# Optimization experiments

Hardware: AMD Instinct MI355X
Metric: run time of the kernel (lower is better)

## Reference

```python
import jax, jax.numpy as jnp
import numpy as np

V = 32000   # vocab
H = 512     # hidden = embed dim
L = 2       # lstm layers
S = 64      # source length
K = 3       # beam width
T = 50      # max decode length
BOS = 1


def lstm_cell(x, h, c, Wih, Whh, b):
    # x,h,c: [B,H]; Wih/Whh: [4H,H]; b: [4H]
    z = x @ Wih.T + h @ Whh.T + b
    i, f, g, o = jnp.split(z, 4, axis=-1)
    c = jax.nn.sigmoid(f) * c + jax.nn.sigmoid(i) * jnp.tanh(g)
    h = jax.nn.sigmoid(o) * jnp.tanh(c)
    return h, c


def run_layer(x, Wih, Whh, b):
    # x: [S,B,H] -> outputs [S,B,H], final h,c [B,H]
    B = x.shape[1]
    z = jnp.zeros((B, H), x.dtype)
    def step(carry, xt):
        h, c = carry
        h, c = lstm_cell(xt, h, c, Wih, Whh, b)
        return (h, c), h
    (h, c), ys = jax.lax.scan(step, (z, z), x)
    return ys, h, c


def setup_inputs() -> dict:
    key = jax.random.key(0)
    ks = jax.random.split(key, 10)
    def p(k, shape, s=0.05):
        return jax.random.normal(k, shape, dtype=jnp.float32) * s
    return {
        'input_seq': jax.random.randint(ks[0], (S, 1), 0, V),
        'emb_enc': p(ks[1], (V, H), 0.1),
        'Wih_enc': p(ks[2], (L, 4 * H, H)),
        'Whh_enc': p(ks[3], (L, 4 * H, H)),
        'b_enc': jnp.zeros((L, 4 * H), jnp.float32),
        'emb_dec': p(ks[4], (V, H), 0.1),
        'Wih_dec': p(ks[5], (L, 4 * H, H)),
        'Whh_dec': p(ks[6], (L, 4 * H, H)),
        'b_dec': jnp.zeros((L, 4 * H), jnp.float32),
        'W_c': p(ks[7], (H, 2 * H)),
        'W_out': p(ks[8], (V, H)),
        'b_out': jnp.zeros((V,), jnp.float32),
        'input_length': S,
        'max_length': T,
        'bos': BOS,
    }


def reference(input_seq, emb_enc, Wih_enc, Whh_enc, b_enc,
              emb_dec, Wih_dec, Whh_dec, b_dec, W_c, W_out, b_out,
              input_length, max_length, bos):
    # ---- encoder ----
    x = emb_enc[input_seq[:, 0]][:, None, :]        # [S,1,H]
    hs, cs = [], []
    for l in range(L):
        x, hl, cl = run_layer(x, Wih_enc[l], Whh_enc[l], b_enc[l])
        hs.append(hl); cs.append(cl)
    enc_out = x[:, 0, :]                            # [S,H]
    h = jnp.stack(hs)                               # [L,1,H]
    c = jnp.stack(cs)

    # ---- decoder single step (vectorized over beam) ----
    def decode_step(tokens, h, c):
        x = emb_dec[tokens]                         # [B,H]
        nh, nc = [], []
        for l in range(L):
            hl, cl = lstm_cell(x, h[l], c[l], Wih_dec[l], Whh_dec[l], b_dec[l])
            nh.append(hl); nc.append(cl); x = hl
        attn = jax.nn.softmax(jnp.einsum('sh,bh->bs', enc_out, x), axis=-1)
        ctx = attn @ enc_out                        # [B,H]
        feat = jnp.tanh(jnp.concatenate([x, ctx], -1) @ W_c.T)
        probs = jax.nn.softmax(feat @ W_out.T + b_out)  # [B,V]
        return probs, jnp.stack(nh), jnp.stack(nc)

    # ---- first step (beam expand) ----
    probs, h, c = decode_step(jnp.array([bos]), h, c)
    topv, topi = jax.lax.top_k(probs[0], K)
    scores = jnp.log(topv)                          # [K]
    tokens = topi                                   # [K]
    h = jnp.repeat(h, K, axis=1)                    # [L,K,H]
    c = jnp.repeat(c, K, axis=1)
    backtrack = jnp.full((K, max_length), bos, dtype=jnp.int32)

    # ---- beam search loop ----
    def body(carry, t):
        tokens, h, c, scores, bt = carry
        probs, hn, cn = decode_step(tokens, h, c)   # [K,V]
        topv, topi = jax.lax.top_k(probs, K)        # [K,K]
        cum = jnp.log(topv) + scores[:, None]
        cand_scores, flat = jax.lax.top_k(cum.reshape(-1), K)
        best = topi.reshape(-1)[flat]
        orig = flat // K                            # beam origins
        bt = bt[orig].at[:, t + 1].set(tokens[orig])
        return (best, hn[:, orig, :], cn[:, orig, :], cand_scores, bt), None

    (tokens, h, c, scores, backtrack), _ = jax.lax.scan(
        body, (tokens, h, c, scores, backtrack), jnp.arange(max_length - 1))
    return backtrack[jnp.argmax(scores)]            # [max_length] tokens
```

## Files before the change

kernel.cpp:

```cpp
#include <hip/hip_runtime.h>
#include <math.h>

#define HSZ   512
#define H4    2048
#define SEQ   64
#define VOC   32000
#define BEAM  3
#define TMAX  50

#define LOFF  ((size_t)H4 * HSZ)

__device__ __forceinline__ float wsum(float v) {
#pragma unroll
  for (int off = 32; off; off >>= 1) v += __shfl_xor(v, off, 64);
  return v;
}
__device__ __forceinline__ float dot4(float4 a, float4 b) {
  return a.x * b.x + a.y * b.y + a.z * b.z + a.w * b.w;
}
__device__ __forceinline__ float sigf(float x) { return 1.f / (1.f + expf(-x)); }

__device__ __forceinline__ bool better(float v1, int i1, float v2, int i2) {
  return (v1 > v2) || (v1 == v2 && i1 < i2);
}
__device__ __forceinline__ void ins3(float* v, int* idx, float nv, int ni) {
  if (better(nv, ni, v[2], idx[2])) {
    if (better(nv, ni, v[1], idx[1])) {
      v[2] = v[1]; idx[2] = idx[1];
      if (better(nv, ni, v[0], idx[0])) { v[1] = v[0]; idx[1] = idx[0]; v[0] = nv; idx[0] = ni; }
      else { v[1] = nv; idx[1] = ni; }
    } else { v[2] = nv; idx[2] = ni; }
  }
}


__global__ void __launch_bounds__(512) k_xw1(const float* __restrict__ Wih,
                                             const float* __restrict__ bias,
                                             const float* __restrict__ emb,
                                             const int* __restrict__ seq,
                                             float* __restrict__ xp1) {
  int t    = threadIdx.x & 63;
  int wave = threadIdx.x >> 6;
  int r    = blockIdx.x * 8 + wave;
  int tok  = seq[t];
  const float* xr = emb + (size_t)tok * HSZ;
  const float* wr = Wih + (size_t)r * HSZ;
  float acc = 0.f;
  for (int e = 0; e < HSZ; e += 4) {
    float4 wv = *(const float4*)(wr + e);
    float4 xv = *(const float4*)(xr + e);
    acc += dot4(wv, xv);
  }
  xp1[t * H4 + r] = acc + bias[r];
}

__global__ void __launch_bounds__(512) k_encslot(const float* __restrict__ Whh1,
                                                 const float* __restrict__ Wih2,
                                                 const float* __restrict__ Whh2,
                                                 const float* __restrict__ b2,
                                                 const float* __restrict__ xp1,
                                                 float* __restrict__ h1a, float* __restrict__ c1a,
                                                 float* __restrict__ h2a, float* __restrict__ c2a,
                                                 int s) {
  __shared__ float rowX[HSZ], rowH[HSZ], zl[16];
  int tid = threadIdx.x, wave = tid >> 6, lane = tid & 63;
  bool l2 = blockIdx.x >= 128;
  int t = l2 ? s - 1 : s;
  if (t < 0 || t >= SEQ) return;
  int bb = blockIdx.x & 127;
  int lr = wave >> 1;
  int j  = bb * 4 + lr;
  int g0 = (wave & 1) * 2;
  if (!l2) {
    rowX[tid] = (t > 0) ? h1a[t * HSZ + tid] : 0.f;
    __syncthreads();
    float4 h0 = ((const float4*)rowX)[lane], h1v = ((const float4*)rowX)[lane + 64];
#pragma unroll
    for (int gg = 0; gg < 2; ++gg) {
      int g = g0 + gg;
      int row = j + (g << 9);
      const float4* wr = (const float4*)(Whh1 + (size_t)row * HSZ);
      float zs = wsum(dot4(wr[lane], h0) + dot4(wr[lane + 64], h1v));
      if (lane == 0) zl[lr * 4 + g] = zs + xp1[t * H4 + row];
    }
    __syncthreads();
    if (tid < 4) {
      int j2 = bb * 4 + tid;
      float z0 = zl[tid * 4 + 0], z1 = zl[tid * 4 + 1], z2 = zl[tid * 4 + 2], z3 = zl[tid * 4 + 3];
      float cp = (t > 0) ? c1a[t * HSZ + j2] : 0.f;
      float c = sigf(z1) * cp + sigf(z0) * tanhf(z2);
      c1a[(t + 1) * HSZ + j2] = c;
      h1a[(t + 1) * HSZ + j2] = sigf(z3) * tanhf(c);
    }
  } else {
    rowX[tid] = h1a[(t + 1) * HSZ + tid];
    rowH[tid] = (t > 0) ? h2a[t * HSZ + tid] : 0.f;
    __syncthreads();
    float4 x0 = ((const float4*)rowX)[lane], x1 = ((const float4*)rowX)[lane + 64];
    float4 h0 = ((const float4*)rowH)[lane], h1v = ((const float4*)rowH)[lane + 64];
#pragma unroll
    for (int gg = 0; gg < 2; ++gg) {
      int g = g0 + gg;
      int row = j + (g << 9);
      const float4* wi = (const float4*)(Wih2 + (size_t)row * HSZ);
      const float4* wh = (const float4*)(Whh2 + (size_t)row * HSZ);
      float zs = wsum(dot4(wi[lane], x0) + dot4(wi[lane + 64], x1) +
                      dot4(wh[lane], h0) + dot4(wh[lane + 64], h1v));
      if (lane == 0) zl[lr * 4 + g] = zs + b2[row];
    }
    __syncthreads();
    if (tid < 4) {
      int j2 = bb * 4 + tid;
      float z0 = zl[tid * 4 + 0], z1 = zl[tid * 4 + 1], z2 = zl[tid * 4 + 2], z3 = zl[tid * 4 + 3];
      float cp = (t > 0) ? c2a[t * HSZ + j2] : 0.f;
      float c = sigf(z1) * cp + sigf(z0) * tanhf(z2);
      c2a[(t + 1) * HSZ + j2] = c;
      h2a[(t + 1) * HSZ + j2] = sigf(z3) * tanhf(c);
    }
  }
}

__global__ void __launch_bounds__(512) k_dinit(const float* __restrict__ h1a,
                                               const float* __restrict__ c1a,
                                               const float* __restrict__ h2a,
                                               const float* __restrict__ c2a,
                                               float* __restrict__ hd, float* __restrict__ cd,
                                               float* __restrict__ x_dec,
                                               const float* __restrict__ emb_dec,
                                               const int* __restrict__ bosp) {
  int bos = bosp[0];
  for (int e = threadIdx.x; e < HSZ; e += 512) {
    hd[e]        = h1a[SEQ * HSZ + e];
    cd[e]        = c1a[SEQ * HSZ + e];
    hd[1536 + e] = h2a[SEQ * HSZ + e];
    cd[1536 + e] = c2a[SEQ * HSZ + e];
    x_dec[e]     = emb_dec[(size_t)bos * HSZ + e];
  }
}


template <int B>
__global__ void __launch_bounds__(512) k_dcell(const float* __restrict__ Wih,
                                               const float* __restrict__ Whh,
                                               const float* __restrict__ bias,
                                               const float* __restrict__ x,
                                               const float* __restrict__ hin,
                                               const float* __restrict__ cin,
                                               float* __restrict__ hout, float* __restrict__ cout) {
  __shared__ float xl[B * HSZ], hl[B * HSZ], cl[B * HSZ], zl[8 * B];
  int tid = threadIdx.x;
  for (int i = tid; i < B * HSZ; i += 512) { xl[i] = x[i]; hl[i] = hin[i]; cl[i] = cin[i]; }
  __syncthreads();
  int wave = tid >> 6, lane = tid & 63;
  int lr = wave >> 2;
  int g  = wave & 3;
  int j  = blockIdx.x * 2 + lr;
  int row = j + (g << 9);
  const float4* wi = (const float4*)(Wih + (size_t)row * HSZ);
  const float4* wh = (const float4*)(Whh + (size_t)row * HSZ);
  float4 wi0 = wi[lane], wi1 = wi[lane + 64], wh0 = wh[lane], wh1 = wh[lane + 64];
  float bb = bias[row];
#pragma unroll
  for (int b = 0; b < B; ++b) {
    float4 xv0 = ((const float4*)(xl + b * HSZ))[lane];
    float4 xv1 = ((const float4*)(xl + b * HSZ))[lane + 64];
    float4 hv0 = ((const float4*)(hl + b * HSZ))[lane];
    float4 hv1 = ((const float4*)(hl + b * HSZ))[lane + 64];
    float acc = dot4(wi0, xv0) + dot4(wi1, xv1) + dot4(wh0, hv0) + dot4(wh1, hv1);
    float z = wsum(acc) + bb;
    if (lane == 0) zl[(lr * 4 + g) * B + b] = z;
  }
  __syncthreads();
  for (int q = tid; q < 2 * B; q += 512) {
    int lr2 = q / B, b = q % B;
    int j2 = blockIdx.x * 2 + lr2;
    float z0 = zl[(lr2 * 4 + 0) * B + b], z1 = zl[(lr2 * 4 + 1) * B + b];
    float z2 = zl[(lr2 * 4 + 2) * B + b], z3 = zl[(lr2 * 4 + 3) * B + b];
    float c = sigf(z1) * cl[b * HSZ + j2] + sigf(z0) * tanhf(z2);
    cout[b * HSZ + j2] = c;
    hout[b * HSZ + j2] = sigf(z3) * tanhf(c);
  }
}

template <int B>
__global__ void __launch_bounds__(512) k_attfeat(const float* __restrict__ h2,
                                                 const float* __restrict__ enc,
                                                 const float* __restrict__ Wc,
                                                 float* __restrict__ feat) {
  __shared__ float xs[BEAM * HSZ], at[BEAM * SEQ], xcs[BEAM * 1024];
  int tid = threadIdx.x;
  for (int i = tid; i < B * HSZ; i += 512) xs[i] = h2[i];
  __syncthreads();
  if (tid < B * SEQ) {
    int b = tid >> 6, s2 = tid & 63;
    const float* er = enc + (s2 + 1) * HSZ;
    const float* xb = xs + b * HSZ;
    float acc = 0.f;
    for (int e = 0; e < HSZ; e += 4) {
      float4 ev = *(const float4*)(er + e);
      acc += ev.x * xb[e] + ev.y * xb[e + 1] + ev.z * xb[e + 2] + ev.w * xb[e + 3];
    }
    at[tid] = acc;
  }
  __syncthreads();
  if (tid < B) {
    float m = -INFINITY;
    for (int s2 = 0; s2 < SEQ; ++s2) m = fmaxf(m, at[tid * SEQ + s2]);
    float s = 0.f;
    for (int s2 = 0; s2 < SEQ; ++s2) { float e = expf(at[tid * SEQ + s2] - m); at[tid * SEQ + s2] = e; s += e; }
    float inv = 1.f / s;
    for (int s2 = 0; s2 < SEQ; ++s2) at[tid * SEQ + s2] *= inv;
  }
  __syncthreads();
  if (tid < 128) {
    int h4 = tid * 4;
    float4 acc[B];
#pragma unroll
    for (int b = 0; b < B; ++b) acc[b] = make_float4(0.f, 0.f, 0.f, 0.f);
    for (int s2 = 0; s2 < SEQ; ++s2) {
      float4 ev = *(const float4*)(enc + (s2 + 1) * HSZ + h4);
#pragma unroll
      for (int b = 0; b < B; ++b) {
        float a = at[b * SEQ + s2];
        acc[b].x += a * ev.x; acc[b].y += a * ev.y; acc[b].z += a * ev.z; acc[b].w += a * ev.w;
      }
    }
#pragma unroll
    for (int b = 0; b < B; ++b) *(float4*)(xcs + b * 1024 + 512 + h4) = acc[b];
  }
  for (int i = tid; i < B * HSZ; i += 512) {
    int b = i >> 9, hcol = i & 511;
    xcs[b * 1024 + hcol] = xs[b * HSZ + hcol];
  }
  __syncthreads();
  int wave = tid >> 6, lane = tid & 63;
  int j = blockIdx.x * 8 + wave;
  const float4* w = (const float4*)(Wc + (size_t)j * 1024);
  float4 w0 = w[lane], w1 = w[lane + 64], w2 = w[lane + 128], w3 = w[lane + 192];
#pragma unroll
  for (int b = 0; b < B; ++b) {
    const float4* xb = (const float4*)(xcs + b * 1024);
    float acc = dot4(w0, xb[lane]) + dot4(w1, xb[lane + 64]) +
                dot4(w2, xb[lane + 128]) + dot4(w3, xb[lane + 192]);
    acc = wsum(acc);
    if (lane == 0) feat[b * HSZ + j] = tanhf(acc);
  }
}

template <int B>
__global__ void __launch_bounds__(512) k_logits(const float* __restrict__ Wout,
                                                const float* __restrict__ bout,
                                                const float* __restrict__ feat,
                                                float* __restrict__ pm, float* __restrict__ ps,
                                                float* __restrict__ pv, int* __restrict__ pi) {
  __shared__ float fst[BEAM * HSZ];
  int tid = threadIdx.x;
  for (int i = tid; i < B * HSZ; i += 512) fst[i] = feat[i];
  __syncthreads();
  int wave = tid >> 6, lane = tid & 63;
  int gid  = blockIdx.x * 8 + wave;
  float4 f0[B], f1[B];
#pragma unroll
  for (int b = 0; b < B; ++b) {
    f0[b] = ((const float4*)(fst + b * HSZ))[lane];
    f1[b] = ((const float4*)(fst + b * HSZ))[lane + 64];
  }
  float m[B], ss[B], tv[B][3];
  int tix[B][3];
#pragma unroll
  for (int b = 0; b < B; ++b) {
    m[b] = -INFINITY; ss[b] = 0.f;
#pragma unroll
    for (int k = 0; k < 3; ++k) { tv[b][k] = -INFINITY; tix[b][k] = 0x7fffffff; }
  }
  for (int k0 = 0; k0 < 16; k0 += 8) {
    float4 a0[8], a1[8]; float ab[8]; int vr[8];
#pragma unroll
    for (int u = 0; u < 8; ++u) {
      int v = gid + (k0 + u) * 2048;
      vr[u] = v;
      if (v < VOC) {
        const float4* wr = (const float4*)(Wout + (size_t)v * HSZ);
        a0[u] = wr[lane]; a1[u] = wr[lane + 64]; ab[u] = bout[v];
      } else {
        a0[u] = make_float4(0.f, 0.f, 0.f, 0.f); a1[u] = a0[u]; ab[u] = 0.f;
      }
    }
#pragma unroll
    for (int u = 0; u < 8; ++u) {
      if (vr[u] >= VOC) continue;
#pragma unroll
      for (int b = 0; b < B; ++b) {
        float acc = wsum(dot4(a0[u], f0[b]) + dot4(a1[u], f1[b])) + ab[u];
        float mo = m[b], mn = fmaxf(mo, acc);
        ss[b] = ss[b] * expf(mo - mn) + expf(acc - mn);
        m[b]  = mn;
        ins3(tv[b], tix[b], acc, vr[u]);
      }
    }
  }
  __shared__ float lm[8][3], lss[8][3], lv[8][3][3];
  __shared__ int li[8][3][3];
  if (lane == 0) {
#pragma unroll
    for (int b = 0; b < B; ++b) {
      lm[wave][b] = m[b]; lss[wave][b] = ss[b];
#pragma unroll
      for (int k = 0; k < 3; ++k) { lv[wave][b][k] = tv[b][k]; li[wave][b][k] = tix[b][k]; }
    }
  }
  __syncthreads();
  if (tid < B) {
    int b = tid;
    float M = -INFINITY;
#pragma unroll
    for (int w2 = 0; w2 < 8; ++w2) M = fmaxf(M, lm[w2][b]);
    float S = 0.f;
#pragma unroll
    for (int w2 = 0; w2 < 8; ++w2) S += lss[w2][b] * expf(lm[w2][b] - M);
    float bv[3] = {-INFINITY, -INFINITY, -INFINITY};
    int bi3[3]  = {0x7fffffff, 0x7fffffff, 0x7fffffff};
#pragma unroll
    for (int w2 = 0; w2 < 8; ++w2)
#pragma unroll
      for (int k = 0; k < 3; ++k) ins3(bv, bi3, lv[w2][b][k], li[w2][b][k]);
    int o = blockIdx.x * 3 + b;
    pm[o] = M; ps[o] = S;
#pragma unroll
    for (int k = 0; k < 3; ++k) { pv[o * 3 + k] = bv[k]; pi[o * 3 + k] = bi3[k]; }
  }
}

template <int B, int STEP0>
__global__ void __launch_bounds__(256) k_merge(const float* __restrict__ pm,
                                               const float* __restrict__ ps,
                                               const float* __restrict__ pv,
                                               const int* __restrict__ pi,
                                               const float* __restrict__ hdn,
                                               const float* __restrict__ cdn,
                                               float* __restrict__ hd, float* __restrict__ cd,
                                               int* __restrict__ bt, float* __restrict__ scores,
                                               int* __restrict__ tokens, float* __restrict__ x_dec,
                                               const float* __restrict__ emb_dec,
                                               const int* __restrict__ bosp,
                                               int* __restrict__ outp, int ti) {
  __shared__ float sM[3], sS[3], sV[3][3], sScore[3];
  __shared__ int sI[3][3], sOrig[3], sTokNew[3], sTokOld[3], sKstar;
  int tid = threadIdx.x, wave = tid >> 6, lane = tid & 63;
  if (wave < B) {
    int b = wave;
    float lm4[4], ls4[4];
    float M = -INFINITY;
#pragma unroll
    for (int q = 0; q < 4; ++q) {
      int blk2 = lane + q * 64;
      lm4[q] = pm[blk2 * 3 + b]; ls4[q] = ps[blk2 * 3 + b];
      M = fmaxf(M, lm4[q]);
    }
#pragma unroll
    for (int off = 32; off; off >>= 1) M = fmaxf(M, __shfl_xor(M, off, 64));
    float S = 0.f;
#pragma unroll
    for (int q = 0; q < 4; ++q) S += ls4[q] * expf(lm4[q] - M);
    S = wsum(S);
    float bv[3] = {-INFINITY, -INFINITY, -INFINITY};
    int bi3[3]  = {0x7fffffff, 0x7fffffff, 0x7fffffff};
#pragma unroll
    for (int q = 0; q < 4; ++q) {
      int blk2 = lane + q * 64;
#pragma unroll
      for (int k = 0; k < 3; ++k)
        ins3(bv, bi3, pv[(blk2 * 3 + b) * 3 + k], pi[(blk2 * 3 + b) * 3 + k]);
    }
#pragma unroll
    for (int off = 32; off; off >>= 1) {
      float ov[3]; int oi[3];
#pragma unroll
      for (int k = 0; k < 3; ++k) { ov[k] = __shfl_xor(bv[k], off, 64); oi[k] = __shfl_xor(bi3[k], off, 64); }
#pragma unroll
      for (int k = 0; k < 3; ++k) ins3(bv, bi3, ov[k], oi[k]);
    }
    if (lane == 0) {
      sM[b] = M; sS[b] = S;
#pragma unroll
      for (int k = 0; k < 3; ++k) { sV[b][k] = bv[k]; sI[b][k] = bi3[k]; }
    }
  }
  __syncthreads();
  if (tid == 0) {
    if (STEP0) {
      float off0 = -sM[0] - logf(sS[0]);
      for (int k = 0; k < 3; ++k) {
        sScore[k] = sV[0][k] + off0;
        sTokNew[k] = sI[0][k]; sOrig[k] = 0; sTokOld[k] = 0;
        scores[k] = sScore[k]; tokens[k] = sTokNew[k];
      }
    } else {
      float osc[3]; int otk[3];
      for (int b = 0; b < 3; ++b) { osc[b] = scores[b]; otk[b] = tokens[b]; sTokOld[b] = otk[b]; }
      float cum[9];
      for (int b = 0; b < 3; ++b) {
        float o = osc[b] - sM[b] - logf(sS[b]);
        for (int k = 0; k < 3; ++k) cum[b * 3 + k] = sV[b][k] + o;
      }
      bool used[9] = {false, false, false, false, false, false, false, false, false};
      for (int k = 0; k < 3; ++k) {
        int bf = 0; float bb = -INFINITY;
        for (int f = 0; f < 9; ++f)
          if (!used[f] && cum[f] > bb) { bb = cum[f]; bf = f; }
        used[bf] = true;
        sScore[k] = bb;
        int ob = bf / 3;
        sOrig[k] = ob;
        sTokNew[k] = sI[ob][bf - ob * 3];
      }
      for (int k = 0; k < 3; ++k) { scores[k] = sScore[k]; tokens[k] = sTokNew[k]; }
    }
    float bb = -INFINITY; int kk = 0;
    for (int k = 0; k < 3; ++k) if (sScore[k] > bb) { bb = sScore[k]; kk = k; }
    sKstar = kk;
  }
  __syncthreads();
  for (int idx = tid; idx < 2 * 3 * HSZ; idx += 256) {
    int l = idx / 1536, rem = idx % 1536, k = rem / HSZ, e = rem & 511;
    int o = STEP0 ? 0 : sOrig[k];
    hd[l * 1536 + k * HSZ + e] = hdn[l * 1536 + o * HSZ + e];
    cd[l * 1536 + k * HSZ + e] = cdn[l * 1536 + o * HSZ + e];
  }
  if (STEP0) {
    int bos = bosp[0];
    for (int idx = tid; idx < BEAM * TMAX; idx += 256) bt[idx] = bos;
  } else {
    const int* src = bt + (ti & 1) * (BEAM * TMAX);
    int* dst = bt + ((ti + 1) & 1) * (BEAM * TMAX);
    for (int idx = tid; idx < BEAM * TMAX; idx += 256) {
      int k = idx / TMAX, jj = idx % TMAX, o = sOrig[k];
      dst[idx] = (jj == ti + 1) ? sTokOld[o] : src[o * TMAX + jj];
    }
  }
  for (int idx = tid; idx < BEAM * HSZ; idx += 256) {
    int k = idx >> 9, e = idx & 511;
    x_dec[idx] = emb_dec[(size_t)sTokNew[k] * HSZ + e];
  }
  if (!STEP0 && ti == TMAX - 2) {
    __syncthreads();
    const int* dst = bt + ((ti + 1) & 1) * (BEAM * TMAX);
    for (int jj = tid; jj < TMAX; jj += 256) outp[jj] = dst[sKstar * TMAX + jj];
  }
}

extern "C" void kernel_launch(void* const* d_in, const int* in_sizes, int n_in,
                              void* d_out, int out_size, void* d_ws, size_t ws_size,
                              hipStream_t stream) {
  const int*   seq     = (const int*)d_in[0];
  const float* emb_enc = (const float*)d_in[1];
  const float* Wih_enc = (const float*)d_in[2];
  const float* Whh_enc = (const float*)d_in[3];
  const float* b_enc   = (const float*)d_in[4];
  const float* emb_dec = (const float*)d_in[5];
  const float* Wih_dec = (const float*)d_in[6];
  const float* Whh_dec = (const float*)d_in[7];
  const float* b_dec   = (const float*)d_in[8];
  const float* W_c     = (const float*)d_in[9];
  const float* W_out   = (const float*)d_in[10];
  const float* b_out   = (const float*)d_in[11];
  const int*   bosp    = (const int*)d_in[14];

  float* w = (float*)d_ws;
  float* xp1     = w; w += SEQ * H4;
  float* h1a     = w; w += (SEQ + 1) * HSZ;
  float* c1a     = w; w += (SEQ + 1) * HSZ;
  float* h2a     = w; w += (SEQ + 1) * HSZ;
  float* c2a     = w; w += (SEQ + 1) * HSZ;
  float* hd      = w; w += 2 * BEAM * HSZ;
  float* cd      = w; w += 2 * BEAM * HSZ;
  float* hdn     = w; w += 2 * BEAM * HSZ;
  float* cdn     = w; w += 2 * BEAM * HSZ;
  float* x_dec   = w; w += BEAM * HSZ;
  float* feat    = w; w += BEAM * HSZ;
  float* pm      = w; w += 256 * 3;
  float* ps      = w; w += 256 * 3;
  float* pv      = w; w += 256 * 3 * 3;
  float* scores  = w; w += 4;
  int* pi     = (int*)w; w += 256 * 3 * 3;
  int* tokens = (int*)w; w += 4;
  int* bt     = (int*)w; w += 2 * BEAM * TMAX + 4;
  int* outp   = (int*)d_out;

  k_xw1<<<256, 512, 0, stream>>>(Wih_enc, b_enc, emb_enc, seq, xp1);
  for (int s = 0; s <= SEQ; ++s)
    k_encslot<<<256, 512, 0, stream>>>(Whh_enc, Wih_enc + LOFF, Whh_enc + LOFF, b_enc + H4,
                                       xp1, h1a, c1a, h2a, c2a, s);
  k_dinit<<<1, 512, 0, stream>>>(h1a, c1a, h2a, c2a, hd, cd, x_dec, emb_dec, bosp);

  for (int step = 0; step < TMAX; ++step) {
    int ti = step - 1;
    if (step == 0) {
      k_dcell<1><<<256, 512, 0, stream>>>(Wih_dec, Whh_dec, b_dec, x_dec, hd, cd, hdn, cdn);
      k_dcell<1><<<256, 512, 0, stream>>>(Wih_dec + LOFF, Whh_dec + LOFF, b_dec + H4,
                                          hdn, hd + 1536, cd + 1536, hdn + 1536, cdn + 1536);
      k_attfeat<1><<<64, 512, 0, stream>>>(hdn + 1536, h2a, W_c, feat);
      k_logits<1><<<256, 512, 0, stream>>>(W_out, b_out, feat, pm, ps, pv, pi);
      k_merge<1, 1><<<1, 256, 0, stream>>>(pm, ps, pv, pi, hdn, cdn, hd, cd, bt, scores,
                                           tokens, x_dec, emb_dec, bosp, outp, ti);
    } else {
      k_dcell<3><<<256, 512, 0, stream>>>(Wih_dec, Whh_dec, b_dec, x_dec, hd, cd, hdn, cdn);
      k_dcell<3><<<256, 512, 0, stream>>>(Wih_dec + LOFF, Whh_dec + LOFF, b_dec + H4,
                                          hdn, hd + 1536, cd + 1536, hdn + 1536, cdn + 1536);
      k_attfeat<3><<<64, 512, 0, stream>>>(hdn + 1536, h2a, W_c, feat);
      k_logits<3><<<256, 512, 0, stream>>>(W_out, b_out, feat, pm, ps, pv, pi);
      k_merge<3, 0><<<1, 256, 0, stream>>>(pm, ps, pv, pi, hdn, cdn, hd, cd, bt, scores,
                                           tokens, x_dec, emb_dec, bosp, outp, ti);
    }
  }
}
```

Measured before the change: 3.897 ms.

## Fuse beam merge/selection into first decoder LSTM cell kernel

Drops the single-block merge kernel and the init kernel. Each of the 256 blocks of the first decoder cell now redoes the top-k merge over the logits partials, then gathers the embeddings and the reordered hidden state directly. Block 0 writes the layer-2 state, the backtrack, the scores and the tokens, using ping-pong buffers to avoid races. This removes one serialized launch per decode step, at the cost of redundant merge work in every block and a new tail kernel for the final step.

```diff
diff --git a/kernel.cpp b/kernel.cpp
--- a/kernel.cpp
+++ b/kernel.cpp
@@ -120,33 +120,174 @@
   }
 }
 
-__global__ void __launch_bounds__(512) k_dinit(const float* __restrict__ h1a,
-                                               const float* __restrict__ c1a,
-                                               const float* __restrict__ h2a,
-                                               const float* __restrict__ c2a,
-                                               float* __restrict__ hd, float* __restrict__ cd,
-                                               float* __restrict__ x_dec,
-                                               const float* __restrict__ emb_dec,
-                                               const int* __restrict__ bosp) {
-  int bos = bosp[0];
-  for (int e = threadIdx.x; e < HSZ; e += 512) {
-    hd[e]        = h1a[SEQ * HSZ + e];
-    cd[e]        = c1a[SEQ * HSZ + e];
-    hd[1536 + e] = h2a[SEQ * HSZ + e];
-    cd[1536 + e] = c2a[SEQ * HSZ + e];
-    x_dec[e]     = emb_dec[(size_t)bos * HSZ + e];
-  }
-}
-
+
+template <int B, int BIN, int MODE>
+__global__ void __launch_bounds__(512) k_dcell1(
+    const float* __restrict__ Wih, const float* __restrict__ Whh,
+    const float* __restrict__ bias,
+    const float* __restrict__ emb_dec, const int* __restrict__ bosp,
+    const float* __restrict__ h1prev, const float* __restrict__ c1prev,
+    const float* __restrict__ h2prev, const float* __restrict__ c2prev,
+    const float* __restrict__ pm, const float* __restrict__ ps,
+    const float* __restrict__ pv, const int* __restrict__ pi,
+    float* __restrict__ hout, float* __restrict__ cout,
+    float* __restrict__ hd2p, float* __restrict__ cd2p,
+    const float* __restrict__ scores_rd, float* __restrict__ scores_wr,
+    const int* __restrict__ tokens_rd, int* __restrict__ tokens_wr,
+    int* __restrict__ bt, int ti) {
+  __shared__ float xl[B * HSZ], hl[B * HSZ], cl[B * HSZ], zl[8 * B];
+  __shared__ float sM[3], sS[3], sV[3][3], sScore[3];
+  __shared__ int sI[3][3], sOrig[3], sTokNew[3], sTokOld[3];
+  int tid = threadIdx.x, wave = tid >> 6, lane = tid & 63;
+
+  if (MODE >= 1) {
+    if (wave < BIN) {
+      int b = wave;
+      float lm4[4], ls4[4];
+      float M = -INFINITY;
+#pragma unroll
+      for (int q = 0; q < 4; ++q) {
+        int blk2 = lane + q * 64;
+        lm4[q] = pm[blk2 * 3 + b]; ls4[q] = ps[blk2 * 3 + b];
+        M = fmaxf(M, lm4[q]);
+      }
+#pragma unroll
+      for (int off = 32; off; off >>= 1) M = fmaxf(M, __shfl_xor(M, off, 64));
+      float S = 0.f;
+#pragma unroll
+      for (int q = 0; q < 4; ++q) S += ls4[q] * expf(lm4[q] - M);
+      S = wsum(S);
+      float bv[3] = {-INFINITY, -INFINITY, -INFINITY};
+      int bi3[3]  = {0x7fffffff, 0x7fffffff, 0x7fffffff};
+#pragma unroll
+      for (int q = 0; q < 4; ++q) {
+        int blk2 = lane + q * 64;
+#pragma unroll
+        for (int k = 0; k < 3; ++k)
+          ins3(bv, bi3, pv[(blk2 * 3 + b) * 3 + k], pi[(blk2 * 3 + b) * 3 + k]);
+      }
+#pragma unroll
+      for (int off = 32; off; off >>= 1) {
+        float ov[3]; int oi[3];
+#pragma unroll
+        for (int k = 0; k < 3; ++k) { ov[k] = __shfl_xor(bv[k], off, 64); oi[k] = __shfl_xor(bi3[k], off, 64); }
+#pragma unroll
+        for (int k = 0; k < 3; ++k) ins3(bv, bi3, ov[k], oi[k]);
+      }
+      if (lane == 0) {
+        sM[b] = M; sS[b] = S;
+#pragma unroll
+        for (int k = 0; k < 3; ++k) { sV[b][k] = bv[k]; sI[b][k] = bi3[k]; }
+      }
+    }
+    __syncthreads();
+    if (tid == 0) {
+      if (MODE == 1) {
+        float off0 = -sM[0] - logf(sS[0]);
+        for (int k = 0; k < 3; ++k) {
+          sScore[k] = sV[0][k] + off0;
+          sTokNew[k] = sI[0][k]; sOrig[k] = 0; sTokOld[k] = 0;
+        }
+      } else {
+        float osc[3];
+        for (int b = 0; b < 3; ++b) { osc[b] = scores_rd[b]; sTokOld[b] = tokens_rd[b]; }
+        float cum[9];
+        for (int b = 0; b < 3; ++b) {
+          float o = osc[b] - sM[b] - logf(sS[b]);
+          for (int k = 0; k < 3; ++k) cum[b * 3 + k] = sV[b][k] + o;
+        }
+        bool used[9] = {false, false, false, false, false, false, false, false, false};
+        for (int k = 0; k < 3; ++k) {
+          int bf = 0; float bb = -INFINITY;
+          for (int f = 0; f < 9; ++f)
+            if (!used[f] && cum[f] > bb) { bb = cum[f]; bf = f; }
+          used[bf] = true;
+          sScore[k] = bb;
+          int ob = bf / 3;
+          sOrig[k] = ob;
+          sTokNew[k] = sI[ob][bf - ob * 3];
+        }
+      }
+    }
+    __syncthreads();
+  }
+
+  if (MODE == 0) {
+    int bos = bosp[0];
+    for (int i = tid; i < B * HSZ; i += 512) {
+      xl[i] = emb_dec[(size_t)bos * HSZ + i];
+      hl[i] = h1prev[i]; cl[i] = c1prev[i];
+    }
+    if (blockIdx.x == 0) {
+      for (int i = tid; i < B * HSZ; i += 512) { hd2p[i] = h2prev[i]; cd2p[i] = c2prev[i]; }
+    }
+  } else {
+    for (int i = tid; i < B * HSZ; i += 512) {
+      int b = i >> 9, e = i & 511;
+      xl[i] = emb_dec[(size_t)sTokNew[b] * HSZ + e];
+      hl[i] = h1prev[sOrig[b] * HSZ + e];
+      cl[i] = c1prev[sOrig[b] * HSZ + e];
+    }
+    if (blockIdx.x == 0) {
+      for (int i = tid; i < B * HSZ; i += 512) {
+        int b = i >> 9, e = i & 511;
+        hd2p[i] = h2prev[sOrig[b] * HSZ + e];
+        cd2p[i] = c2prev[sOrig[b] * HSZ + e];
+      }
+      if (MODE == 1) {
+        int bos = bosp[0];
+        for (int idx = tid; idx < BEAM * TMAX; idx += 512) bt[idx] = bos;
+      } else {
+        const int* src = bt + (ti & 1) * (BEAM * TMAX);
+        int* dst = bt + ((ti + 1) & 1) * (BEAM * TMAX);
+        for (int idx = tid; idx < BEAM * TMAX; idx += 512) {
+          int k = idx / TMAX, jj = idx % TMAX, o = sOrig[k];
+          dst[idx] = (jj == ti + 1) ? sTokOld[o] : src[o * TMAX + jj];
+        }
+      }
+      if (tid < 3) { scores_wr[tid] = sScore[tid]; tokens_wr[tid] = sTokNew[tid]; }
+    }
+  }
+  __syncthreads();
+
+  int lr = wave >> 2;
+  int g  = wave & 3;
+  int j  = blockIdx.x * 2 + lr;
+  int row = j + (g << 9);
+  const float4* wi = (const float4*)(Wih + (size_t)row * HSZ);
+  const float4* wh = (const float4*)(Whh + (size_t)row * HSZ);
+  float4 wi0 = wi[lane], wi1 = wi[lane + 64], wh0 = wh[lane], wh1 = wh[lane + 64];
+  float bb = bias[row];
+#pragma unroll
+  for (int b = 0; b < B; ++b) {
+    float4 xv0 = ((const float4*)(xl + b * HSZ))[lane];
+    float4 xv1 = ((const float4*)(xl + b * HSZ))[lane + 64];
+    float4 hv0 = ((const float4*)(hl + b * HSZ))[lane];
+    float4 hv1 = ((const float4*)(hl + b * HSZ))[lane + 64];
+    float acc = dot4(wi0, xv0) + dot4(wi1, xv1) + dot4(wh0, hv0) + dot4(wh1, hv1);
+    float z = wsum(acc) + bb;
+    if (lane == 0) zl[(lr * 4 + g) * B + b] = z;
+  }
+  __syncthreads();
+  for (int q = tid; q < 2 * B; q += 512) {
+    int lr2 = q / B, b = q % B;
+    int j2 = blockIdx.x * 2 + lr2;
+    float z0 = zl[(lr2 * 4 + 0) * B + b], z1 = zl[(lr2 * 4 + 1) * B + b];
+    float z2 = zl[(lr2 * 4 + 2) * B + b], z3 = zl[(lr2 * 4 + 3) * B + b];
+    float c = sigf(z1) * cl[b * HSZ + j2] + sigf(z0) * tanhf(z2);
+    cout[b * HSZ + j2] = c;
+    hout[b * HSZ + j2] = sigf(z3) * tanhf(c);
+  }
+}
 
 template <int B>
-__global__ void __launch_bounds__(512) k_dcell(const float* __restrict__ Wih,
-                                               const float* __restrict__ Whh,
-                                               const float* __restrict__ bias,
-                                               const float* __restrict__ x,
-                                               const float* __restrict__ hin,
-                                               const float* __restrict__ cin,
-                                               float* __restrict__ hout, float* __restrict__ cout) {
+__global__ void __launch_bounds__(512) k_dcell2(const float* __restrict__ Wih,
+                                                const float* __restrict__ Whh,
+                                                const float* __restrict__ bias,
+                                                const float* __restrict__ x,
+                                                const float* __restrict__ hin,
+                                                const float* __restrict__ cin,
+                                                float* __restrict__ hout, float* __restrict__ cout) {
   __shared__ float xl[B * HSZ], hl[B * HSZ], cl[B * HSZ], zl[8 * B];
   int tid = threadIdx.x;
   for (int i = tid; i < B * HSZ; i += 512) { xl[i] = x[i]; hl[i] = hin[i]; cl[i] = cin[i]; }
@@ -331,23 +472,18 @@
   }
 }
 
-template <int B, int STEP0>
-__global__ void __launch_bounds__(256) k_merge(const float* __restrict__ pm,
-                                               const float* __restrict__ ps,
-                                               const float* __restrict__ pv,
-                                               const int* __restrict__ pi,
-                                               const float* __restrict__ hdn,
-                                               const float* __restrict__ cdn,
-                                               float* __restrict__ hd, float* __restrict__ cd,
-                                               int* __restrict__ bt, float* __restrict__ scores,
-                                               int* __restrict__ tokens, float* __restrict__ x_dec,
-                                               const float* __restrict__ emb_dec,
-                                               const int* __restrict__ bosp,
-                                               int* __restrict__ outp, int ti) {
+__global__ void __launch_bounds__(256) k_tail(const float* __restrict__ pm,
+                                              const float* __restrict__ ps,
+                                              const float* __restrict__ pv,
+                                              const int* __restrict__ pi,
+                                              const float* __restrict__ scores_rd,
+                                              const int* __restrict__ tokens_rd,
+                                              int* __restrict__ bt, int* __restrict__ outp) {
+  const int ti = TMAX - 2;
   __shared__ float sM[3], sS[3], sV[3][3], sScore[3];
-  __shared__ int sI[3][3], sOrig[3], sTokNew[3], sTokOld[3], sKstar;
+  __shared__ int sI[3][3], sOrig[3], sTokOld[3], sKstar;
   int tid = threadIdx.x, wave = tid >> 6, lane = tid & 63;
-  if (wave < B) {
+  if (wave < 3) {
     int b = wave;
     float lm4[4], ls4[4];
     float M = -INFINITY;
@@ -388,65 +524,35 @@
   }
   __syncthreads();
   if (tid == 0) {
-    if (STEP0) {
-      float off0 = -sM[0] - logf(sS[0]);
-      for (int k = 0; k < 3; ++k) {
-        sScore[k] = sV[0][k] + off0;
-        sTokNew[k] = sI[0][k]; sOrig[k] = 0; sTokOld[k] = 0;
-        scores[k] = sScore[k]; tokens[k] = sTokNew[k];
-      }
-    } else {
-      float osc[3]; int otk[3];
-      for (int b = 0; b < 3; ++b) { osc[b] = scores[b]; otk[b] = tokens[b]; sTokOld[b] = otk[b]; }
-      float cum[9];
-      for (int b = 0; b < 3; ++b) {
-        float o = osc[b] - sM[b] - logf(sS[b]);
-        for (int k = 0; k < 3; ++k) cum[b * 3 + k] = sV[b][k] + o;
-      }
-      bool used[9] = {false, false, false, false, false, false, false, false, false};
-      for (int k = 0; k < 3; ++k) {
-        int bf = 0; float bb = -INFINITY;
-        for (int f = 0; f < 9; ++f)
-          if (!used[f] && cum[f] > bb) { bb = cum[f]; bf = f; }
-        used[bf] = true;
-        sScore[k] = bb;
-        int ob = bf / 3;
-        sOrig[k] = ob;
-        sTokNew[k] = sI[ob][bf - ob * 3];
-      }
-      for (int k = 0; k < 3; ++k) { scores[k] = sScore[k]; tokens[k] = sTokNew[k]; }
+    float osc[3];
+    for (int b = 0; b < 3; ++b) { osc[b] = scores_rd[b]; sTokOld[b] = tokens_rd[b]; }
+    float cum[9];
+    for (int b = 0; b < 3; ++b) {
+      float o = osc[b] - sM[b] - logf(sS[b]);
+      for (int k = 0; k < 3; ++k) cum[b * 3 + k] = sV[b][k] + o;
+    }
+    bool used[9] = {false, false, false, false, false, false, false, false, false};
+    for (int k = 0; k < 3; ++k) {
+      int bf = 0; float bb = -INFINITY;
+      for (int f = 0; f < 9; ++f)
+        if (!used[f] && cum[f] > bb) { bb = cum[f]; bf = f; }
+      used[bf] = true;
+      sScore[k] = bb;
+      sOrig[k] = bf / 3;
     }
     float bb = -INFINITY; int kk = 0;
     for (int k = 0; k < 3; ++k) if (sScore[k] > bb) { bb = sScore[k]; kk = k; }
     sKstar = kk;
   }
   __syncthreads();
-  for (int idx = tid; idx < 2 * 3 * HSZ; idx += 256) {
-    int l = idx / 1536, rem = idx % 1536, k = rem / HSZ, e = rem & 511;
-    int o = STEP0 ? 0 : sOrig[k];
-    hd[l * 1536 + k * HSZ + e] = hdn[l * 1536 + o * HSZ + e];
-    cd[l * 1536 + k * HSZ + e] = cdn[l * 1536 + o * HSZ + e];
-  }
-  if (STEP0) {
-    int bos = bosp[0];
-    for (int idx = tid; idx < BEAM * TMAX; idx += 256) bt[idx] = bos;
-  } else {
-    const int* src = bt + (ti & 1) * (BEAM * TMAX);
-    int* dst = bt + ((ti + 1) & 1) * (BEAM * TMAX);
-    for (int idx = tid; idx < BEAM * TMAX; idx += 256) {
-      int k = idx / TMAX, jj = idx % TMAX, o = sOrig[k];
-      dst[idx] = (jj == ti + 1) ? sTokOld[o] : src[o * TMAX + jj];
-    }
-  }
-  for (int idx = tid; idx < BEAM * HSZ; idx += 256) {
-    int k = idx >> 9, e = idx & 511;
-    x_dec[idx] = emb_dec[(size_t)sTokNew[k] * HSZ + e];
-  }
-  if (!STEP0 && ti == TMAX - 2) {
-    __syncthreads();
-    const int* dst = bt + ((ti + 1) & 1) * (BEAM * TMAX);
-    for (int jj = tid; jj < TMAX; jj += 256) outp[jj] = dst[sKstar * TMAX + jj];
-  }
+  const int* src = bt + (ti & 1) * (BEAM * TMAX);
+  int* dst = bt + ((ti + 1) & 1) * (BEAM * TMAX);
+  for (int idx = tid; idx < BEAM * TMAX; idx += 256) {
+    int k = idx / TMAX, jj = idx % TMAX, o = sOrig[k];
+    dst[idx] = (jj == ti + 1) ? sTokOld[o] : src[o * TMAX + jj];
+  }
+  __syncthreads();
+  for (int jj = tid; jj < TMAX; jj += 256) outp[jj] = dst[sKstar * TMAX + jj];
 }
 
 extern "C" void kernel_launch(void* const* d_in, const int* in_sizes, int n_in,
@@ -472,18 +578,19 @@
   float* c1a     = w; w += (SEQ + 1) * HSZ;
   float* h2a     = w; w += (SEQ + 1) * HSZ;
   float* c2a     = w; w += (SEQ + 1) * HSZ;
-  float* hd      = w; w += 2 * BEAM * HSZ;
-  float* cd      = w; w += 2 * BEAM * HSZ;
-  float* hdn     = w; w += 2 * BEAM * HSZ;
-  float* cdn     = w; w += 2 * BEAM * HSZ;
-  float* x_dec   = w; w += BEAM * HSZ;
+  float* hdn1    = w; w += 2 * BEAM * HSZ;
+  float* cdn1    = w; w += 2 * BEAM * HSZ;
+  float* hdn2    = w; w += 2 * BEAM * HSZ;
+  float* cdn2    = w; w += 2 * BEAM * HSZ;
+  float* hd2p    = w; w += BEAM * HSZ;
+  float* cd2p    = w; w += BEAM * HSZ;
   float* feat    = w; w += BEAM * HSZ;
   float* pm      = w; w += 256 * 3;
   float* ps      = w; w += 256 * 3;
   float* pv      = w; w += 256 * 3 * 3;
-  float* scores  = w; w += 4;
+  float* sb      = w; w += 2 * 4;
   int* pi     = (int*)w; w += 256 * 3 * 3;
-  int* tokens = (int*)w; w += 4;
+  int* tb     = (int*)w; w += 2 * 4;
   int* bt     = (int*)w; w += 2 * BEAM * TMAX + 4;
   int* outp   = (int*)d_out;
 
@@ -491,26 +598,42 @@
   for (int s = 0; s <= SEQ; ++s)
     k_encslot<<<256, 512, 0, stream>>>(Whh_enc, Wih_enc + LOFF, Whh_enc + LOFF, b_enc + H4,
                                        xp1, h1a, c1a, h2a, c2a, s);
-  k_dinit<<<1, 512, 0, stream>>>(h1a, c1a, h2a, c2a, hd, cd, x_dec, emb_dec, bosp);
-
-  for (int step = 0; step < TMAX; ++step) {
-    int ti = step - 1;
-    if (step == 0) {
-      k_dcell<1><<<256, 512, 0, stream>>>(Wih_dec, Whh_dec, b_dec, x_dec, hd, cd, hdn, cdn);
-      k_dcell<1><<<256, 512, 0, stream>>>(Wih_dec + LOFF, Whh_dec + LOFF, b_dec + H4,
-                                          hdn, hd + 1536, cd + 1536, hdn + 1536, cdn + 1536);
-      k_attfeat<1><<<64, 512, 0, stream>>>(hdn + 1536, h2a, W_c, feat);
+
+  for (int s = 0; s < TMAX; ++s) {
+    int rp = (s - 1) & 1, wp = s & 1;
+    if (s == 0) {
+      k_dcell1<1, 1, 0><<<256, 512, 0, stream>>>(
+          Wih_dec, Whh_dec, b_dec, emb_dec, bosp,
+          h1a + SEQ * HSZ, c1a + SEQ * HSZ, h2a + SEQ * HSZ, c2a + SEQ * HSZ,
+          pm, ps, pv, pi,
+          hdn1 + 0, cdn1 + 0, hd2p, cd2p,
+          sb, sb, tb, tb, bt, 0);
+      k_dcell2<1><<<256, 512, 0, stream>>>(Wih_dec + LOFF, Whh_dec + LOFF, b_dec + H4,
+                                           hdn1 + 0, hd2p, cd2p, hdn2 + 0, cdn2 + 0);
+      k_attfeat<1><<<64, 512, 0, stream>>>(hdn2 + 0, h2a, W_c, feat);
       k_logits<1><<<256, 512, 0, stream>>>(W_out, b_out, feat, pm, ps, pv, pi);
-      k_merge<1, 1><<<1, 256, 0, stream>>>(pm, ps, pv, pi, hdn, cdn, hd, cd, bt, scores,
-                                           tokens, x_dec, emb_dec, bosp, outp, ti);
     } else {
-      k_dcell<3><<<256, 512, 0, stream>>>(Wih_dec, Whh_dec, b_dec, x_dec, hd, cd, hdn, cdn);
-      k_dcell<3><<<256, 512, 0, stream>>>(Wih_dec + LOFF, Whh_dec + LOFF, b_dec + H4,
-                                          hdn, hd + 1536, cd + 1536, hdn + 1536, cdn + 1536);
-      k_attfeat<3><<<64, 512, 0, stream>>>(hdn + 1536, h2a, W_c, feat);
+      float* h1p = hdn1 + rp * BEAM * HSZ; float* c1p = cdn1 + rp * BEAM * HSZ;
+      float* h2p = hdn2 + rp * BEAM * HSZ; float* c2p = cdn2 + rp * BEAM * HSZ;
+      float* h1o = hdn1 + wp * BEAM * HSZ; float* c1o = cdn1 + wp * BEAM * HSZ;
+      float* h2o = hdn2 + wp * BEAM * HSZ; float* c2o = cdn2 + wp * BEAM * HSZ;
+      if (s == 1)
+        k_dcell1<3, 1, 1><<<256, 512, 0, stream>>>(
+            Wih_dec, Whh_dec, b_dec, emb_dec, bosp,
+            h1p, c1p, h2p, c2p, pm, ps, pv, pi,
+            h1o, c1o, hd2p, cd2p,
+            sb + rp * 4, sb + wp * 4, tb + rp * 4, tb + wp * 4, bt, -1);
+      else
+        k_dcell1<3, 3, 2><<<256, 512, 0, stream>>>(
+            Wih_dec, Whh_dec, b_dec, emb_dec, bosp,
+            h1p, c1p, h2p, c2p, pm, ps, pv, pi,
+            h1o, c1o, hd2p, cd2p,
+            sb + rp * 4, sb + wp * 4, tb + rp * 4, tb + wp * 4, bt, s - 2);
+      k_dcell2<3><<<256, 512, 0, stream>>>(Wih_dec + LOFF, Whh_dec + LOFF, b_dec + H4,
+                                           h1o, hd2p, cd2p, h2o, c2o);
+      k_attfeat<3><<<64, 512, 0, stream>>>(h2o, h2a, W_c, feat);
       k_logits<3><<<256, 512, 0, stream>>>(W_out, b_out, feat, pm, ps, pv, pi);
-      k_merge<3, 0><<<1, 256, 0, stream>>>(pm, ps, pv, pi, hdn, cdn, hd, cd, bt, scores,
-                                           tokens, x_dec, emb_dec, bosp, outp, ti);
-    }
-  }
-}
+    }
+  }
+  k_tail<<<1, 256, 0, stream>>>(pm, ps, pv, pi, sb + 4, tb + 4, bt, outp);
+}
```

Result: faster. 3.595 ms (-7.7%).
